# Kernel tuning notes

Hardware: AMD Instinct MI355X
Metric: run time of the kernel (lower is better)

Reference implementation:

```python
import jax, jax.numpy as jnp
import numpy as np

# MyConvT config (matches init_kwargs)
K, S, P, OP = 5, 2, 2, 1  # kernel, stride, padding, output_padding


def setup_inputs() -> dict:
    key = jax.random.key(0)
    k0, k1, k2, k3 = jax.random.split(key, 4)
    B, Cin, Cout, H, W = 8, 192, 128, 64, 64
    OH = (H - 1) * S + K - 2 * P + OP  # 128
    OW = (W - 1) * S + K - 2 * P + OP  # 128
    x = jax.random.normal(k0, (B, Cin, H, W), jnp.float32)
    # mask spatial must be (OH + K - 1, OW + K - 1) so its unfold has OH*OW columns
    mask = jax.random.randint(k1, (B, 1, OH + K - 1, OW + K - 1), 0, 2, jnp.int32)
    # torch ConvTranspose2d weight layout: [in_channels, out_channels, kH, kW]
    weight = jax.random.normal(k2, (Cin, Cout, K, K), jnp.float32) * 0.05
    bias = jax.random.normal(k3, (Cout,), jnp.float32) * 0.05
    return {"x": x, "mask": mask, "weight": weight, "bias": bias}


def _masked_conv_transpose(x, mask, weight, bias):
    # The torch module does: zero-insert (stride dilation), pad (K-1-P each side,
    # plus OP trailing), unfold, gather valid patches (where the unfolded mask
    # patch has any nonzero), dense matmul with rot180/transposed weight + bias,
    # then masked_scatter back (zeros elsewhere). Mathematically:
    #   out = mask_any * (conv_transpose2d(x, weight) + bias)
    # where mask_any[b,oh,ow] = any(mask[b,:, oh:oh+K, ow:ow+K] != 0).
    kern = jnp.flip(weight, (2, 3)).transpose(1, 0, 2, 3)  # -> OIHW correlation kernel
    pad = ((K - 1 - P, K - 1 - P + OP), (K - 1 - P, K - 1 - P + OP))
    y = jax.lax.conv_general_dilated(
        x, kern, window_strides=(1, 1), padding=pad, lhs_dilation=(S, S),
        dimension_numbers=("NCHW", "OIHW", "NCHW"))  # [B, Cout, OH, OW]
    m = (mask != 0).astype(y.dtype)  # [B, 1, OH+K-1, OW+K-1]
    pooled = jax.lax.reduce_window(m, 0.0, jax.lax.max,
                                   (1, 1, K, K), (1, 1, 1, 1), "VALID")  # [B,1,OH,OW]
    return jnp.where(pooled > 0, y + bias[None, :, None, None], 0.0)


def reference(x, mask, weight, bias):
    return _masked_conv_transpose(x, mask, weight, bias)
```

## Files before the change

### kernel.cpp

```cpp
#include <hip/hip_runtime.h>


#define NB   8
#define CIN  192
#define COUT 128
#define HH   64
#define OHH  128
#define OWW  128
#define MH   132
#define MW   132

#define X4_IYH_B 27648
#define PLANE_B  9216
#define XBUF_B   36864
#define WOFF     36864
#define NSLOT    5
#define LDS_B    (XBUF_B + NSLOT * 8192)

typedef short bf16x8 __attribute__((ext_vector_type(8)));
typedef float f32x4  __attribute__((ext_vector_type(4)));
typedef float f32x2  __attribute__((ext_vector_type(2)));

static __device__ __forceinline__ unsigned short f2bf(float f) {
  union { float f; unsigned int u; } a; a.f = f;
  return (unsigned short)((a.u + 0x7fffu + ((a.u >> 16) & 1u)) >> 16);
}

#define GLOAD_LDS16(gp, lp) __builtin_amdgcn_global_load_lds(                      \
    (const __attribute__((address_space(1))) void*)(gp),                           \
    (__attribute__((address_space(3))) void*)(lp), 16, 0, 0)

__global__ __launch_bounds__(256) void pool_mask_k(const int* __restrict__ mask,
                                                   unsigned char* __restrict__ many) {
  int idx = blockIdx.x * 256 + threadIdx.x;
  if (idx >= NB * OHH * OWW) return;
  int ow = idx & (OWW - 1);
  int oh = (idx >> 7) & (OHH - 1);
  int b  = idx >> 14;
  const int* mp = mask + (b * MH + oh) * MW + ow;
  int any = 0;
  #pragma unroll
  for (int i = 0; i < 5; ++i)
    #pragma unroll
    for (int j = 0; j < 5; ++j)
      any |= mp[i * MW + j];
  many[idx] = (any != 0) ? 1 : 0;
}

__global__ __launch_bounds__(256) void xpose_k(const float* __restrict__ x,
                                               unsigned short* __restrict__ x4) {
  const int b = blockIdx.x / 66, iyH = blockIdx.x % 66;
  const int lane = threadIdx.x & 63, wv = threadIdx.x >> 6;
  unsigned short* pl = x4 + (size_t)(b * 66 + iyH) * (X4_IYH_B / 2);

  if (iyH == 0 || iyH == 65) {
    for (int i = threadIdx.x; i < X4_IYH_B / 16; i += 256)
      *(uint4*)(pl + i * 8) = make_uint4(0, 0, 0, 0);
    return;
  }
  const int iy = iyH - 1;
  if (threadIdx.x < 48) {
    int c3 = threadIdx.x >> 4, rr = (threadIdx.x >> 3) & 1, ch = threadIdx.x & 7;
    *(uint4*)(pl + (c3 * 72 + rr * 65) * 64 + ch * 8) = make_uint4(0, 0, 0, 0);
  }
  #pragma unroll
  for (int k = 0; k < 6; ++k) {
    int ci0 = wv * 48 + k * 8;
    int c3 = ci0 >> 6, cr = ci0 & 63;
    unsigned short p[8];
    #pragma unroll
    for (int e = 0; e < 8; ++e)
      p[e] = f2bf(x[(((size_t)b * CIN + ci0 + e) * HH + iy) * HH + lane]);
    uint4 v;
    v.x = (unsigned)p[0] | ((unsigned)p[1] << 16);
    v.y = (unsigned)p[2] | ((unsigned)p[3] << 16);
    v.z = (unsigned)p[4] | ((unsigned)p[5] << 16);
    v.w = (unsigned)p[6] | ((unsigned)p[7] << 16);
    *(uint4*)(pl + ((size_t)c3 * 72 + 1 + lane) * 64 + cr) = v;
  }
}

__global__ __launch_bounds__(256) void wpack_k(const float* __restrict__ w,
                                               unsigned short* __restrict__ w4) {
  int idx = blockIdx.x * 256 + threadIdx.x;
  if (idx >= CIN * COUT) return;
  int ci = idx % CIN, co = idx / CIN;
  int cob = co >> 6, c = co & 63, c3 = ci >> 6, cir = ci & 63;
  const float* src = w + (size_t)(ci * COUT + co) * 25;
  #pragma unroll
  for (int tap = 0; tap < 25; ++tap)
    w4[(size_t)((tap * 2 + cob) * 3 + c3) * 4096 + c * 64 + cir] = f2bf(src[tap]);
}

__global__ __launch_bounds__(256, 2) void convt_mfma(
    const unsigned short* __restrict__ x4, const unsigned short* __restrict__ w4,
    const float* __restrict__ bias, const unsigned char* __restrict__ many,
    float* __restrict__ out) {
  __shared__ char lds[LDS_B];
  constexpr int TKH[25] = {0,0,1,1, 0,0,1,1, 0,1, 2,2,3,3, 2,2,3,3, 2,3, 4,4, 4,4, 4};
  constexpr int TKW[25] = {0,1,0,1, 2,3,2,3, 4,4, 0,1,0,1, 2,3,2,3, 4,4, 0,1, 2,3, 4};
  constexpr int TNG[25] = {1,0,0,0, 1,0,0,0, 1,0, 1,0,0,0, 1,0,0,0, 1,0, 1,0, 1,0, 1};

  const int tid = threadIdx.x, lane = tid & 63, wv = tid >> 6;
  const int l15 = lane & 15, kc = lane >> 4;
  const int cos = wv & 1, oyr = wv >> 1;
  const int b = blockIdx.x & 7, qq = blockIdx.x >> 3;
  const int cob = qq & 1, oyq = qq >> 1;
  const int oy0 = oyq * 2, oy = oy0 + oyr;
  const int sswz = (lane >> 3) * 128 + (((lane & 7) ^ (lane >> 3)) << 4);

  const char* x4b = (const char*)x4 + (size_t)(b * 66 + oy0) * X4_IYH_B;
  const char* w4b = (const char*)w4 + cob * 24576;

  f32x4 acc[2][2][2][4];
  #pragma unroll
  for (int p = 0; p < 2; ++p)
    #pragma unroll
    for (int q2 = 0; q2 < 2; ++q2)
      #pragma unroll
      for (int i = 0; i < 2; ++i)
        #pragma unroll
        for (int j = 0; j < 4; ++j)
          acc[p][q2][i][j] = (f32x4){0.f, 0.f, 0.f, 0.f};

  auto stage_x = [&](int c3) {
    #pragma unroll
    for (int j = 0; j < 9; ++j) {
      int qc = wv + 4 * j;
      int p = qc / 9, ch = qc % 9;
      GLOAD_LDS16(x4b + (size_t)p * X4_IYH_B + c3 * PLANE_B + ch * 1024 + sswz,
                  lds + p * PLANE_B + ch * 1024 + lane * 16);
    }
  };
  auto stage_w = [&](int tap, int c3, int slot) {
    const char* s = w4b + (size_t)(TKH[tap] * 5 + TKW[tap]) * 49152 + c3 * 8192
                    + wv * 2048 + sswz;
    char* d = lds + WOFF + slot * 8192 + wv * 2048 + lane * 16;
    GLOAD_LDS16(s, d);
    GLOAD_LDS16(s + 1024, d + 1024);
  };

  stage_x(0);
  stage_w(0, 0, 0);
  stage_w(1, 0, 1);
  stage_w(2, 0, 2);
  asm volatile("s_waitcnt vmcnt(4)" ::: "memory");
  __builtin_amdgcn_s_barrier();

  bf16x8 bfr[2][4], afr[2][2];
  #pragma unroll 1
  for (int c3 = 0; c3 < 3; ++c3) {
    #pragma unroll
    for (int t = 0; t < 25; ++t) {
      if (c3 < 2 || t < 22) {
        const int tn = (t + 3 < 25) ? t + 3 : t - 22;
        const int cn = (t + 3 < 25) ? c3 : c3 + 1;
        stage_w(tn, cn, (t + 3) % 5);
      }
      if (c3 == 2 && t >= 22) {
        if (t == 22)      asm volatile("s_waitcnt vmcnt(4)" ::: "memory");
        else if (t == 23) asm volatile("s_waitcnt vmcnt(2)" ::: "memory");
        else              asm volatile("s_waitcnt vmcnt(0)" ::: "memory");
      } else {
        asm volatile("s_waitcnt vmcnt(6)" ::: "memory");
      }
      __builtin_amdgcn_s_barrier();
      if (TNG[t]) {
        const int kj = TKW[t] >> 1, kk = TKH[t] >> 1;
        const int p = oyr + 2 - kk;
        #pragma unroll
        for (int k2 = 0; k2 < 2; ++k2)
          #pragma unroll
          for (int ti = 0; ti < 4; ++ti) {
            const int row = ti * 16 + l15 + 2 - kj;
            bfr[k2][ti] = *(const bf16x8*)(lds + p * PLANE_B + row * 128 +
                                           (((k2 * 4 + kc) ^ (row & 7)) << 4));
          }
      }
      const char* ws = lds + WOFF + (t % 5) * 8192;
      #pragma unroll
      for (int k2 = 0; k2 < 2; ++k2)
        #pragma unroll
        for (int mi = 0; mi < 2; ++mi) {
          const int row = cos * 32 + mi * 16 + l15;
          afr[k2][mi] = *(const bf16x8*)(ws + row * 128 +
                                         (((k2 * 4 + kc) ^ (l15 & 7)) << 4));
        }
      const int ph = TKH[t] & 1, pw = TKW[t] & 1;
      __builtin_amdgcn_s_setprio(1);
      #pragma unroll
      for (int k2 = 0; k2 < 2; ++k2)
        #pragma unroll
        for (int mi = 0; mi < 2; ++mi)
          #pragma unroll
          for (int ti = 0; ti < 4; ++ti)
            acc[ph][pw][mi][ti] = __builtin_amdgcn_mfma_f32_16x16x32_bf16(
                afr[k2][mi], bfr[k2][ti], acc[ph][pw][mi][ti], 0, 0, 0);
      __builtin_amdgcn_s_setprio(0);
    }
    if (c3 < 2) {
      __builtin_amdgcn_s_barrier();
      stage_x(c3 + 1);
      asm volatile("s_waitcnt vmcnt(0)" ::: "memory");
      __builtin_amdgcn_s_barrier();
    }
  }

  const int cobase = cob * 64 + cos * 32;
  #pragma unroll
  for (int mi = 0; mi < 2; ++mi) {
    const f32x4 bv = *(const f32x4*)(bias + cobase + mi * 16 + kc * 4);
    #pragma unroll
    for (int ph = 0; ph < 2; ++ph) {
      const int oh = 2 * oy + ph;
      const unsigned char* mrow = many + ((size_t)b * OHH + oh) * OWW;
      #pragma unroll
      for (int ti = 0; ti < 4; ++ti) {
        const int ow0 = 2 * (ti * 16 + l15);
        const unsigned short m2 = *(const unsigned short*)(mrow + ow0);
        #pragma unroll
        for (int r = 0; r < 4; ++r) {
          const int co = cobase + mi * 16 + kc * 4 + r;
          f32x2 v;
          v.x = (m2 & 0x00FFu) ? acc[ph][0][mi][ti][r] + bv[r] : 0.f;
          v.y = (m2 & 0xFF00u) ? acc[ph][1][mi][ti][r] + bv[r] : 0.f;
          *(f32x2*)(out + (((size_t)(b * COUT + co)) * OHH + oh) * OWW + ow0) = v;
        }
      }
    }
  }
}

extern "C" void kernel_launch(void* const* d_in, const int* in_sizes, int n_in,
                              void* d_out, int out_size, void* d_ws, size_t ws_size,
                              hipStream_t stream) {
  const float* x    = (const float*)d_in[0];
  const int*   mask = (const int*)d_in[1];
  const float* w    = (const float*)d_in[2];
  const float* bias = (const float*)d_in[3];
  float* out = (float*)d_out;

  unsigned char*  many = (unsigned char*)d_ws;
  unsigned short* x4   = (unsigned short*)((char*)d_ws + 131072);
  unsigned short* w4   = (unsigned short*)((char*)d_ws + 131072 +
                                           (size_t)NB * 66 * X4_IYH_B);

  pool_mask_k<<<(NB * OHH * OWW + 255) / 256, 256, 0, stream>>>(mask, many);
  xpose_k<<<NB * 66, 256, 0, stream>>>(x, x4);
  wpack_k<<<(CIN * COUT + 255) / 256, 256, 0, stream>>>(w, w4);
  convt_mfma<<<512, 256, 0, stream>>>(x4, w4, bias, many, out);
}
```

Measured before the change: 62.99 us.

## Fuse prep kernels into one launch and double-buffer B fragments across taps

Merges the mask pooling, input transpose and weight packing kernels into a single launch, removing two kernel launches and their gaps. The mask pooling now handles four outputs per thread with vector loads. The main loop is fully unrolled by hand with double-buffered B-fragment registers, so the next tap group's LDS reads are issued before the current MFMAs rather than after a barrier. This raises register pressure, and the tap-to-phase table is now hand-written, which adds a risk of indexing mistakes.

```diff
diff --git a/kernel.cpp b/kernel.cpp
--- a/kernel.cpp
+++ b/kernel.cpp
@@ -30,76 +30,122 @@
     (const __attribute__((address_space(1))) void*)(gp),                           \
     (__attribute__((address_space(3))) void*)(lp), 16, 0, 0)
 
-__global__ __launch_bounds__(256) void pool_mask_k(const int* __restrict__ mask,
-                                                   unsigned char* __restrict__ many) {
-  int idx = blockIdx.x * 256 + threadIdx.x;
-  if (idx >= NB * OHH * OWW) return;
-  int ow = idx & (OWW - 1);
-  int oh = (idx >> 7) & (OHH - 1);
-  int b  = idx >> 14;
-  const int* mp = mask + (b * MH + oh) * MW + ow;
-  int any = 0;
-  #pragma unroll
-  for (int i = 0; i < 5; ++i)
-    #pragma unroll
-    for (int j = 0; j < 5; ++j)
-      any |= mp[i * MW + j];
-  many[idx] = (any != 0) ? 1 : 0;
-}
-
-__global__ __launch_bounds__(256) void xpose_k(const float* __restrict__ x,
-                                               unsigned short* __restrict__ x4) {
-  const int b = blockIdx.x / 66, iyH = blockIdx.x % 66;
-  const int lane = threadIdx.x & 63, wv = threadIdx.x >> 6;
-  unsigned short* pl = x4 + (size_t)(b * 66 + iyH) * (X4_IYH_B / 2);
-
-  if (iyH == 0 || iyH == 65) {
-    for (int i = threadIdx.x; i < X4_IYH_B / 16; i += 256)
-      *(uint4*)(pl + i * 8) = make_uint4(0, 0, 0, 0);
-    return;
+__global__ __launch_bounds__(256) void prep_k(
+    const float* __restrict__ x, const int* __restrict__ mask,
+    const float* __restrict__ w, unsigned short* __restrict__ x4,
+    unsigned short* __restrict__ w4, unsigned char* __restrict__ many) {
+  const int bid = blockIdx.x, tid = threadIdx.x;
+
+  if (bid < 528) {
+    const int b = bid / 66, iyH = bid % 66;
+    const int lane = tid & 63, wv = tid >> 6;
+    unsigned short* pl = x4 + (size_t)(b * 66 + iyH) * (X4_IYH_B / 2);
+
+    if (iyH == 0 || iyH == 65) {
+      for (int i = tid; i < X4_IYH_B / 16; i += 256)
+        *(uint4*)(pl + i * 8) = make_uint4(0, 0, 0, 0);
+      return;
+    }
+    const int iy = iyH - 1;
+    if (tid < 48) {
+      int c3 = tid >> 4, rr = (tid >> 3) & 1, ch = tid & 7;
+      *(uint4*)(pl + (c3 * 72 + rr * 65) * 64 + ch * 8) = make_uint4(0, 0, 0, 0);
+    }
+    #pragma unroll
+    for (int k = 0; k < 6; ++k) {
+      int ci0 = wv * 48 + k * 8;
+      int c3 = ci0 >> 6, cr = ci0 & 63;
+      unsigned short p[8];
+      #pragma unroll
+      for (int e = 0; e < 8; ++e)
+        p[e] = f2bf(x[(((size_t)b * CIN + ci0 + e) * HH + iy) * HH + lane]);
+      uint4 v;
+      v.x = (unsigned)p[0] | ((unsigned)p[1] << 16);
+      v.y = (unsigned)p[2] | ((unsigned)p[3] << 16);
+      v.z = (unsigned)p[4] | ((unsigned)p[5] << 16);
+      v.w = (unsigned)p[6] | ((unsigned)p[7] << 16);
+      *(uint4*)(pl + ((size_t)c3 * 72 + 1 + lane) * 64 + cr) = v;
+    }
+  } else if (bid < 624) {
+    int idx = (bid - 528) * 256 + tid;
+    int ci = idx % CIN, co = idx / CIN;
+    int cob = co >> 6, c = co & 63, c3 = ci >> 6, cir = ci & 63;
+    const float* src = w + (size_t)(ci * COUT + co) * 25;
+    #pragma unroll
+    for (int tap = 0; tap < 25; ++tap)
+      w4[(size_t)((tap * 2 + cob) * 3 + c3) * 4096 + c * 64 + cir] = f2bf(src[tap]);
+  } else {
+    int g = (bid - 624) * 256 + tid;
+    int owq = g & 31, oh = (g >> 5) & 127, b = g >> 12;
+    const int* mp = mask + (b * MH + oh) * MW + owq * 4;
+    int a0 = 0, a1 = 0, a2 = 0, a3 = 0;
+    #pragma unroll
+    for (int i = 0; i < 5; ++i) {
+      int4 u = *(const int4*)(mp + i * MW);
+      int4 v = *(const int4*)(mp + i * MW + 4);
+      int c = u.z | u.w | v.x;
+      a0 |= u.x | u.y | c;
+      a1 |= u.y | c | v.y;
+      a2 |= c | v.y | v.z;
+      a3 |= u.w | v.x | v.y | v.z | v.w;
+    }
+    *(uchar4*)(many + ((size_t)b * OHH + oh) * OWW + owq * 4) =
+        make_uchar4(a0 ? 1 : 0, a1 ? 1 : 0, a2 ? 1 : 0, a3 ? 1 : 0);
   }
-  const int iy = iyH - 1;
-  if (threadIdx.x < 48) {
-    int c3 = threadIdx.x >> 4, rr = (threadIdx.x >> 3) & 1, ch = threadIdx.x & 7;
-    *(uint4*)(pl + (c3 * 72 + rr * 65) * 64 + ch * 8) = make_uint4(0, 0, 0, 0);
-  }
-  #pragma unroll
-  for (int k = 0; k < 6; ++k) {
-    int ci0 = wv * 48 + k * 8;
-    int c3 = ci0 >> 6, cr = ci0 & 63;
-    unsigned short p[8];
-    #pragma unroll
-    for (int e = 0; e < 8; ++e)
-      p[e] = f2bf(x[(((size_t)b * CIN + ci0 + e) * HH + iy) * HH + lane]);
-    uint4 v;
-    v.x = (unsigned)p[0] | ((unsigned)p[1] << 16);
-    v.y = (unsigned)p[2] | ((unsigned)p[3] << 16);
-    v.z = (unsigned)p[4] | ((unsigned)p[5] << 16);
-    v.w = (unsigned)p[6] | ((unsigned)p[7] << 16);
-    *(uint4*)(pl + ((size_t)c3 * 72 + 1 + lane) * 64 + cr) = v;
-  }
-}
-
-__global__ __launch_bounds__(256) void wpack_k(const float* __restrict__ w,
-                                               unsigned short* __restrict__ w4) {
-  int idx = blockIdx.x * 256 + threadIdx.x;
-  if (idx >= CIN * COUT) return;
-  int ci = idx % CIN, co = idx / CIN;
-  int cob = co >> 6, c = co & 63, c3 = ci >> 6, cir = ci & 63;
-  const float* src = w + (size_t)(ci * COUT + co) * 25;
-  #pragma unroll
-  for (int tap = 0; tap < 25; ++tap)
-    w4[(size_t)((tap * 2 + cob) * 3 + c3) * 4096 + c * 64 + cir] = f2bf(src[tap]);
-}
+}
+
+__constant__ const int TKH[25] = {0,0,1,1, 0,0,1,1, 0,1, 2,2,3,3, 2,2,3,3, 2,3, 4,4, 4,4, 4};
+__constant__ const int TKW[25] = {0,1,0,1, 2,3,2,3, 4,4, 0,1,0,1, 2,3,2,3, 4,4, 0,1, 2,3, 4};
+
+#define BF_LOAD(S, KK, KJ)                                                     \
+  { const int p_ = oyr + 2 - (KK);                                             \
+    _Pragma("unroll") for (int k2 = 0; k2 < 2; ++k2)                           \
+      _Pragma("unroll") for (int ti = 0; ti < 4; ++ti) {                       \
+        const int row_ = ti * 16 + l15 + 2 - (KJ);                             \
+        bfr[S][k2][ti] = *(const bf16x8*)(lds + p_ * PLANE_B + row_ * 128 +    \
+                                          (((k2 * 4 + kc) ^ (row_ & 7)) << 4)); } }
+
+#define AF_LOAD(T)                                                             \
+  { const char* ws_ = lds + WOFF + ((T) % 5) * 8192;                           \
+    _Pragma("unroll") for (int k2 = 0; k2 < 2; ++k2)                           \
+      _Pragma("unroll") for (int mi = 0; mi < 2; ++mi) {                       \
+        const int row_ = cos * 32 + mi * 16 + l15;                             \
+        afr[k2][mi] = *(const bf16x8*)(ws_ + row_ * 128 +                      \
+                                       (((k2 * 4 + kc) ^ (l15 & 7)) << 4)); } }
+
+#define SG(T)                                                                  \
+  { if (c3 < 2 || (T) < 22) {                                                  \
+      const int tn_ = ((T) + 3 < 25) ? (T) + 3 : (T) - 22;                     \
+      const int cn_ = ((T) + 3 < 25) ? c3 : c3 + 1;                            \
+      stage_w(TKH[tn_] * 5 + TKW[tn_], cn_, ((T) + 3) % 5);                    \
+    }                                                                          \
+    if (c3 == 2 && (T) >= 22) {                                                \
+      if ((T) == 22)      asm volatile("s_waitcnt vmcnt(4)" ::: "memory");     \
+      else if ((T) == 23) asm volatile("s_waitcnt vmcnt(2)" ::: "memory");     \
+      else                asm volatile("s_waitcnt vmcnt(0)" ::: "memory");     \
+    } else {                                                                   \
+      asm volatile("s_waitcnt vmcnt(6)" ::: "memory");                         \
+    }                                                                          \
+    __builtin_amdgcn_s_barrier(); }
+
+#define MM(S, PH_, PW_)                                                        \
+  { __builtin_amdgcn_s_setprio(1);                                             \
+    _Pragma("unroll") for (int k2 = 0; k2 < 2; ++k2)                           \
+      _Pragma("unroll") for (int mi = 0; mi < 2; ++mi)                         \
+        _Pragma("unroll") for (int ti = 0; ti < 4; ++ti)                       \
+          acc[PH_][PW_][mi][ti] = __builtin_amdgcn_mfma_f32_16x16x32_bf16(     \
+              afr[k2][mi], bfr[S][k2][ti], acc[PH_][PW_][mi][ti], 0, 0, 0);    \
+    __builtin_amdgcn_s_setprio(0); }
+
+#define TAP(T, PH_, PW_, S)        { SG(T) AF_LOAD(T) MM(S, PH_, PW_) }
+#define TAPP(T, PH_, PW_, S, KK, KJ) \
+  { SG(T) AF_LOAD(T) BF_LOAD((S) ^ 1, KK, KJ) MM(S, PH_, PW_) }
 
 __global__ __launch_bounds__(256, 2) void convt_mfma(
     const unsigned short* __restrict__ x4, const unsigned short* __restrict__ w4,
     const float* __restrict__ bias, const unsigned char* __restrict__ many,
     float* __restrict__ out) {
-  __shared__ char lds[LDS_B];
-  constexpr int TKH[25] = {0,0,1,1, 0,0,1,1, 0,1, 2,2,3,3, 2,2,3,3, 2,3, 4,4, 4,4, 4};
-  constexpr int TKW[25] = {0,1,0,1, 2,3,2,3, 4,4, 0,1,0,1, 2,3,2,3, 4,4, 0,1, 2,3, 4};
-  constexpr int TNG[25] = {1,0,0,0, 1,0,0,0, 1,0, 1,0,0,0, 1,0,0,0, 1,0, 1,0, 1,0, 1};
+  __shared__ __align__(16) char lds[LDS_B];
 
   const int tid = threadIdx.x, lane = tid & 63, wv = tid >> 6;
   const int l15 = lane & 15, kc = lane >> 4;
@@ -132,9 +178,8 @@
                   lds + p * PLANE_B + ch * 1024 + lane * 16);
     }
   };
-  auto stage_w = [&](int tap, int c3, int slot) {
-    const char* s = w4b + (size_t)(TKH[tap] * 5 + TKW[tap]) * 49152 + c3 * 8192
-                    + wv * 2048 + sswz;
+  auto stage_w = [&](int tapid, int c3n, int slot) {
+    const char* s = w4b + (size_t)tapid * 49152 + c3n * 8192 + wv * 2048 + sswz;
     char* d = lds + WOFF + slot * 8192 + wv * 2048 + lane * 16;
     GLOAD_LDS16(s, d);
     GLOAD_LDS16(s + 1024, d + 1024);
@@ -143,61 +188,31 @@
   stage_x(0);
   stage_w(0, 0, 0);
   stage_w(1, 0, 1);
-  stage_w(2, 0, 2);
+  stage_w(5, 0, 2);
   asm volatile("s_waitcnt vmcnt(4)" ::: "memory");
   __builtin_amdgcn_s_barrier();
 
-  bf16x8 bfr[2][4], afr[2][2];
+  bf16x8 bfr[2][2][4], afr[2][2];
   #pragma unroll 1
   for (int c3 = 0; c3 < 3; ++c3) {
-    #pragma unroll
-    for (int t = 0; t < 25; ++t) {
-      if (c3 < 2 || t < 22) {
-        const int tn = (t + 3 < 25) ? t + 3 : t - 22;
-        const int cn = (t + 3 < 25) ? c3 : c3 + 1;
-        stage_w(tn, cn, (t + 3) % 5);
-      }
-      if (c3 == 2 && t >= 22) {
-        if (t == 22)      asm volatile("s_waitcnt vmcnt(4)" ::: "memory");
-        else if (t == 23) asm volatile("s_waitcnt vmcnt(2)" ::: "memory");
-        else              asm volatile("s_waitcnt vmcnt(0)" ::: "memory");
-      } else {
-        asm volatile("s_waitcnt vmcnt(6)" ::: "memory");
-      }
-      __builtin_amdgcn_s_barrier();
-      if (TNG[t]) {
-        const int kj = TKW[t] >> 1, kk = TKH[t] >> 1;
-        const int p = oyr + 2 - kk;
-        #pragma unroll
-        for (int k2 = 0; k2 < 2; ++k2)
-          #pragma unroll
-          for (int ti = 0; ti < 4; ++ti) {
-            const int row = ti * 16 + l15 + 2 - kj;
-            bfr[k2][ti] = *(const bf16x8*)(lds + p * PLANE_B + row * 128 +
-                                           (((k2 * 4 + kc) ^ (row & 7)) << 4));
-          }
-      }
-      const char* ws = lds + WOFF + (t % 5) * 8192;
-      #pragma unroll
-      for (int k2 = 0; k2 < 2; ++k2)
-        #pragma unroll
-        for (int mi = 0; mi < 2; ++mi) {
-          const int row = cos * 32 + mi * 16 + l15;
-          afr[k2][mi] = *(const bf16x8*)(ws + row * 128 +
-                                         (((k2 * 4 + kc) ^ (l15 & 7)) << 4));
-        }
-      const int ph = TKH[t] & 1, pw = TKW[t] & 1;
-      __builtin_amdgcn_s_setprio(1);
-      #pragma unroll
-      for (int k2 = 0; k2 < 2; ++k2)
-        #pragma unroll
-        for (int mi = 0; mi < 2; ++mi)
-          #pragma unroll
-          for (int ti = 0; ti < 4; ++ti)
-            acc[ph][pw][mi][ti] = __builtin_amdgcn_mfma_f32_16x16x32_bf16(
-                afr[k2][mi], bfr[k2][ti], acc[ph][pw][mi][ti], 0, 0, 0);
-      __builtin_amdgcn_s_setprio(0);
-    }
+    BF_LOAD(0, 0, 0)
+    TAP (0,  0, 0, 0) TAP (1,  0, 1, 0) TAP (2,  1, 0, 0)
+    TAPP(3,  1, 1, 0, 0, 1)
+    TAP (4,  0, 0, 1) TAP (5,  0, 1, 1) TAP (6,  1, 0, 1)
+    TAPP(7,  1, 1, 1, 0, 2)
+    TAP (8,  0, 0, 0)
+    TAPP(9,  1, 0, 0, 1, 0)
+    TAP (10, 0, 0, 1) TAP (11, 0, 1, 1) TAP (12, 1, 0, 1)
+    TAPP(13, 1, 1, 1, 1, 1)
+    TAP (14, 0, 0, 0) TAP (15, 0, 1, 0) TAP (16, 1, 0, 0)
+    TAPP(17, 1, 1, 0, 1, 2)
+    TAP (18, 0, 0, 1)
+    TAPP(19, 1, 0, 1, 2, 0)
+    TAP (20, 0, 0, 0)
+    TAPP(21, 0, 1, 0, 2, 1)
+    TAP (22, 0, 0, 1)
+    TAPP(23, 0, 1, 1, 2, 2)
+    TAP (24, 0, 0, 0)
     if (c3 < 2) {
       __builtin_amdgcn_s_barrier();
       stage_x(c3 + 1);
@@ -245,8 +260,6 @@
   unsigned short* w4   = (unsigned short*)((char*)d_ws + 131072 +
                                            (size_t)NB * 66 * X4_IYH_B);
 
-  pool_mask_k<<<(NB * OHH * OWW + 255) / 256, 256, 0, stream>>>(mask, many);
-  xpose_k<<<NB * 66, 256, 0, stream>>>(x, x4);
-  wpack_k<<<(CIN * COUT + 255) / 256, 256, 0, stream>>>(w, w4);
+  prep_k<<<752, 256, 0, stream>>>(x, mask, w, x4, w4, many);
   convt_mfma<<<512, 256, 0, stream>>>(x4, w4, bias, many, out);
 }
```

New measurement: 61.08 us. 3.0% less time.
